# Kernel tuning notes

Hardware: AMD Instinct MI355X
Metric: run time of the kernel (lower is better)

Reference implementation:

```python
import jax, jax.numpy as jnp
import numpy as np

B, H, LB, PW, TC = 4096, 64, 32, 16, 1
WL = LB + PW  # window_length = look_back + prediction


def setup_inputs() -> dict:
    key = jax.random.key(0)
    ks = jax.random.split(key, 9)
    bnd = 1.0 / np.sqrt(H)  # torch Linear default init bound
    bnd_h = 1.0 / np.sqrt(H)
    return {
        "x": jax.random.normal(ks[0], (B, LB, TC), jnp.float32),
        "F_w": jax.random.uniform(ks[1], (WL, H, H), jnp.float32, -bnd, bnd),
        "F_b": jax.random.uniform(ks[2], (WL, H), jnp.float32, -bnd, bnd),
        "H_w": jax.random.uniform(ks[3], (WL, TC, H), jnp.float32, -bnd_h, bnd_h),
        "H_b": jax.random.uniform(ks[4], (WL, TC), jnp.float32, -bnd_h, bnd_h),
        "initial_state": jax.random.normal(ks[5], (H,), jnp.float32),
        "initial_covariance": 0.1 * jax.random.normal(ks[6], (H, H), jnp.float32),
        "Q": 0.1 * jax.random.normal(ks[7], (H, H), jnp.float32),
        "R": jnp.eye(TC, dtype=jnp.float32) + 0.1 * jax.random.normal(ks[8], (TC, TC), jnp.float32),
    }


def _kalman_forward(x, F_w, F_b, H_w, H_b, s0, P0, Q, R):
    nb = x.shape[0]
    hs = jnp.broadcast_to(s0, (nb, H))          # (B,H)
    P = jnp.broadcast_to(P0, (nb, H, H))        # (B,H,H)
    ys = jnp.moveaxis(x[:, :LB, :TC], 0, 1)     # (LB,B,TC) per-step observations

    @jax.checkpoint
    def kf_step(carry, inp):
        hs, P = carry
        Fw, Fb, Hw, Hb, y = inp
        hs_pred = hs @ Fw.T + Fb                                        # (B,H)
        P_pred = jnp.einsum('ij,bjk,lk->bil', Fw, P, Fw) + Q            # F P F^T + Q
        resid = y - (hs_pred @ Hw.T + Hb)                               # (B,TC)
        S = jnp.einsum('ij,bjk,lk->bil', Hw, P_pred, Hw) + R            # (B,TC,TC)
        K = jnp.einsum('bij,kj->bik', P_pred, Hw) @ jnp.linalg.inv(S)   # (B,H,TC)
        hs_new = hs_pred + jnp.einsum('bij,bj->bi', K, resid)
        P_new = P_pred - jnp.einsum('bit,tj,bjk->bik', K, Hw, P_pred)   # (I-KH)P_pred
        return (hs_new, P_new), None

    (hs, _), _ = jax.lax.scan(
        kf_step, (hs, P), (F_w[:LB], F_b[:LB], H_w[:LB], H_b[:LB], ys))

    def pred_step(hs, inp):
        Fw, Fb, Hw, Hb = inp
        hs = hs @ Fw.T + Fb
        return hs, hs @ Hw.T + Hb

    _, ems = jax.lax.scan(
        pred_step, hs, (F_w[LB:], F_b[LB:], H_w[LB:], H_b[LB:]))  # (PW,B,TC)
    # torch.cat(preds, dim=1).unsqueeze(-1) -> (B, PW*TC, 1)
    return jnp.moveaxis(ems, 0, 1).reshape(nb, PW * TC)[..., None]


def reference(x, F_w, F_b, H_w, H_b, initial_state, initial_covariance, Q, R):
    return _kalman_forward(x, F_w, F_b, H_w, H_b, initial_state, initial_covariance, Q, R)
```

## Files before the change

kernel.cpp:

```cpp
#include <hip/hip_runtime.h>


constexpr int KP_OFF = 0;
constexpr int WP_OFF = 2048;
constexpr int UP_OFF = 4160;
constexpr int EP_OFF = 5184;
constexpr int CNT_OFF = 5200;
constexpr int WS_U64 = 5201;

typedef float    f32x4 __attribute__((ext_vector_type(4)));
typedef _Float16 f16x4 __attribute__((ext_vector_type(4)));

#define MFMA16(a, b, c) __builtin_amdgcn_mfma_f32_16x16x16f16((a), (b), (c), 0, 0, 0)

template <int CTRL>
__device__ __forceinline__ float dpp_add(float x) {
  int v = __builtin_amdgcn_update_dpp(0, __builtin_bit_cast(int, x), CTRL, 0xf, 0xf, true);
  return x + __builtin_bit_cast(float, v);
}
__device__ __forceinline__ float sum16(float x) {
  x = dpp_add<0xB1>(x);
  x = dpp_add<0x4E>(x);
  x = dpp_add<0x141>(x);
  x = dpp_add<0x140>(x);
  return x;
}

__device__ __forceinline__ float spin_read(const unsigned long long* p, unsigned tag) {
  unsigned long long v = 0;
  for (int it = 0; it < (1 << 22); ++it) {
    v = __hip_atomic_load(p, __ATOMIC_RELAXED, __HIP_MEMORY_SCOPE_AGENT);
    if ((unsigned)(v >> 32) == tag) break;
  }
  union { unsigned u; float f; } cv; cv.u = (unsigned)v;
  return cv.f;
}
__device__ __forceinline__ float spin_read_sleep(const unsigned long long* p, unsigned tag) {
  unsigned long long v = 0;
  for (int it = 0; it < (1 << 20); ++it) {
    v = __hip_atomic_load(p, __ATOMIC_RELAXED, __HIP_MEMORY_SCOPE_AGENT);
    if ((unsigned)(v >> 32) == tag) break;
    __builtin_amdgcn_s_sleep(2);
  }
  union { unsigned u; float f; } cv; cv.u = (unsigned)v;
  return cv.f;
}
__device__ __forceinline__ void pub_write(unsigned long long* p, unsigned tag, float x) {
  union { float f; unsigned u; } cv; cv.f = x;
  __hip_atomic_store(p, ((unsigned long long)tag << 32) | cv.u,
                     __ATOMIC_RELAXED, __HIP_MEMORY_SCOPE_AGENT);
}
__device__ __forceinline__ void lds_barrier() {
  asm volatile("s_waitcnt lgkmcnt(0)" ::: "memory");
  __builtin_amdgcn_sched_barrier(0);
  __builtin_amdgcn_s_barrier();
  __builtin_amdgcn_sched_barrier(0);
}

__global__ __launch_bounds__(512) void kalman_fused(
    const float* __restrict__ Fw, const float* __restrict__ Fb,
    const float* __restrict__ Hw, const float* __restrict__ Hb,
    const float* __restrict__ s0, const float* __restrict__ P0,
    const float* __restrict__ Qg, const float* __restrict__ Rg,
    const float* __restrict__ x, float* __restrict__ out,
    unsigned long long* __restrict__ ws) {
  __shared__ __align__(16) char smem[43008];
  const int tid  = threadIdx.x;
  const int lane = tid & 63;
  const int w    = tid >> 6;
  const int blk  = blockIdx.x;
  unsigned long long* kp = ws + KP_OFF;
  unsigned long long* wp = ws + WP_OFF;
  unsigned long long* up = ws + UP_OFF;
  unsigned long long* ep = ws + EP_OFF;

  if (blk == 0) {
    _Float16* FFh = (_Float16*)smem;
    _Float16* TF  = (_Float16*)(smem + 8192);
    float*    PF  = (float*)(smem + 16384);
    float*    Hws = (float*)(smem + 32768);
    float*    nred = (float*)(smem + 40960);
    float*    mred = (float*)(smem + 41472);
    float*    Sred = (float*)(smem + 42496);

    const int l15 = lane & 15, g = lane >> 4;
    const int ti = w >> 1, half = w & 1;
    const int tj0 = 2 * half, tj1 = 2 * half + 1;
    const int sr = tid >> 3, sc0 = (tid & 7) * 8;
    const int fi0 = (sr >> 4) * 4 + (sc0 >> 4);
    const int L0  = (sr & 15) + 16 * ((sc0 & 15) >> 2);
    const float R0 = Rg[0];

    auto stageFh = [&](f32x4 a, f32x4 b) {
      f16x4 pa, pb;
      #pragma unroll
      for (int u = 0; u < 4; ++u) { pa[u] = (_Float16)a[u]; pb[u] = (_Float16)b[u]; }
      *(f16x4*)&FFh[(fi0 * 64 + L0) * 4]      = pa;
      *(f16x4*)&FFh[(fi0 * 64 + L0 + 16) * 4] = pb;
    };

    f32x4 qf0, qf1;
    #pragma unroll
    for (int reg = 0; reg < 4; ++reg) {
      qf0[reg] = Qg[(16 * ti + 4 * g + reg) * 64 + 16 * tj0 + l15];
      qf1[reg] = Qg[(16 * ti + 4 * g + reg) * 64 + 16 * tj1 + l15];
    }
    for (int idx = tid; idx < 2048; idx += 512) Hws[idx] = Hw[idx];
    #pragma unroll
    for (int s = 0; s < 2; ++s) {
      const int slot = tid + s * 512;
      const int f = slot >> 6, ln = slot & 63;
      const int a = f >> 2, b = f & 3, g2 = ln >> 4, l2 = ln & 15;
      f32x4 v;
      #pragma unroll
      for (int r = 0; r < 4; ++r)
        v[r] = P0[(16 * a + 4 * g2 + r) * 64 + 16 * b + l2];
      *(f32x4*)&PF[(f * 64 + ln) * 4] = v;
    }
    {
      f32x4 a = *(const f32x4*)(Fw + sr * 64 + sc0);
      f32x4 b = *(const f32x4*)(Fw + sr * 64 + sc0 + 4);
      stageFh(a, b);
    }
    for (int idx = tid; idx < 2 * 64; idx += 512) nred[idx] = 0.f;
    for (int idx = tid; idx < 4 * 64; idx += 512) mred[idx] = 0.f;
    if (tid < 8) Sred[tid] = 0.f;
    __syncthreads();

    f32x4 fna, fnb;
    for (int t = 0; t < 32; ++t) {
      if (t + 1 < 32) {
        fna = *(const f32x4*)(Fw + (size_t)(t + 1) * 4096 + sr * 64 + sc0);
        fnb = *(const f32x4*)(Fw + (size_t)(t + 1) * 4096 + sr * 64 + sc0 + 4);
      }
      float S;
      {
        const f32x4 sa = *(const f32x4*)&Sred[0];
        const f32x4 sb = *(const f32x4*)&Sred[4];
        S = ((sa.x + sa.y) + (sa.z + sa.w)) + ((sb.x + sb.y) + (sb.z + sb.w));
      }
      const float rcpS = 1.0f / (S + R0);
      const int ia = 16 * ti + l15;
      const float hPl = mred[ia] + mred[64 + ia] + mred[128 + ia] + mred[192 + ia];

      f16x4 Ah[4], Al[4];
      #pragma unroll
      for (int kc = 0; kc < 4; ++kc) {
        const int na = 16 * kc + 4 * g;
        const f32x4 n4 = *(const f32x4*)&nred[na] + *(const f32x4*)&nred[64 + na];
        const f32x4 k4 = n4 * rcpS;
        const f32x4 p4 = *(const f32x4*)&PF[((kc * 4 + ti) * 64 + lane) * 4] - k4 * hPl;
        #pragma unroll
        for (int j = 0; j < 4; ++j) {
          const _Float16 h_ = (_Float16)p4[j];
          Ah[kc][j] = h_;
          Al[kc][j] = (_Float16)((p4[j] - (float)h_) * 2048.0f);
        }
      }
      f16x4 Bf[2][4];
      #pragma unroll
      for (int s2 = 0; s2 < 2; ++s2) {
        const int tj = tj0 + s2;
        #pragma unroll
        for (int kc = 0; kc < 4; ++kc)
          Bf[s2][kc] = *(const f16x4*)&FFh[((tj * 4 + kc) * 64 + lane) * 4];
      }
      if (w == 0 && t > 0) {
        const float kl = (nred[lane] + nred[64 + lane]) * rcpS;
        pub_write(&kp[(t - 1) * 64 + lane], (unsigned)t, kl);
      }
      #pragma unroll
      for (int s2 = 0; s2 < 2; ++s2) {
        const int tj = tj0 + s2;
        f32x4 am = {0.f, 0.f, 0.f, 0.f}, a2 = {0.f, 0.f, 0.f, 0.f};
        #pragma unroll
        for (int kc = 0; kc < 4; ++kc) {
          am = MFMA16(Ah[kc], Bf[s2][kc], am);
          a2 = MFMA16(Al[kc], Bf[s2][kc], a2);
        }
        const f32x4 uv = am + a2 * (1.0f / 2048.0f);
        f16x4 uh;
        #pragma unroll
        for (int j = 0; j < 4; ++j) uh[j] = (_Float16)uv[j];
        *(f16x4*)&TF[((ti * 4 + tj) * 64 + lane) * 4] = uh;
      }
      lds_barrier();

      if (t + 1 < 32) stageFh(fna, fnb);
      f16x4 Ua[4];
      #pragma unroll
      for (int kc = 0; kc < 4; ++kc)
        Ua[kc] = *(const f16x4*)&TF[((kc * 4 + ti) * 64 + lane) * 4];
      f32x4 pout[2];
      #pragma unroll
      for (int s2 = 0; s2 < 2; ++s2) {
        const int tj = tj0 + s2;
        f32x4 acc = {0.f, 0.f, 0.f, 0.f};
        #pragma unroll
        for (int kc = 0; kc < 4; ++kc) acc = MFMA16(Ua[kc], Bf[s2][kc], acc);
        acc += (s2 ? qf1 : qf0);
        pout[s2] = acc;
        *(f32x4*)&PF[((ti * 4 + tj) * 64 + lane) * 4] = acc;
      }
      const float hcA = Hws[t * 64 + 16 * tj0 + l15];
      const float hcB = Hws[t * 64 + 16 * tj1 + l15];
      const f32x4 h4 = *(const f32x4*)&Hws[t * 64 + 16 * ti + 4 * g];
      const f32x4 npv = pout[0] * hcA + pout[1] * hcB;
      const float np0 = sum16(npv.x), np1 = sum16(npv.y);
      const float np2 = sum16(npv.z), np3 = sum16(npv.w);
      float sel = np0;
      sel = (l15 == 1) ? np1 : sel;
      sel = (l15 == 2) ? np2 : sel;
      sel = (l15 == 3) ? np3 : sel;
      if (l15 < 4) nred[half * 64 + 16 * ti + 4 * g + l15] = sel;
      float mp0 = pout[0].x * h4.x + pout[0].y * h4.y + pout[0].z * h4.z + pout[0].w * h4.w;
      float mp1 = pout[1].x * h4.x + pout[1].y * h4.y + pout[1].z * h4.z + pout[1].w * h4.w;
      mp0 += __shfl_xor(mp0, 16, 64); mp0 += __shfl_xor(mp0, 32, 64);
      mp1 += __shfl_xor(mp1, 16, 64); mp1 += __shfl_xor(mp1, 32, 64);
      if (g == 0) {
        mred[ti * 64 + 16 * tj0 + l15] = mp0;
        mred[ti * 64 + 16 * tj1 + l15] = mp1;
      }
      float sp = npv.x * h4.x + npv.y * h4.y + npv.z * h4.z + npv.w * h4.w;
      sp = sum16(sp);
      sp += __shfl_xor(sp, 16, 64); sp += __shfl_xor(sp, 32, 64);
      if (lane == 0) Sred[w] = sp;
      lds_barrier();
    }
    if (w == 0) {
      const f32x4 sa = *(const f32x4*)&Sred[0];
      const f32x4 sb = *(const f32x4*)&Sred[4];
      const float S = ((sa.x + sa.y) + (sa.z + sa.w)) + ((sb.x + sb.y) + (sb.z + sb.w));
      const float kl = (nred[lane] + nred[64 + lane]) / (S + R0);
      pub_write(&kp[31 * 64 + lane], 32u, kl);
    }
    return;
  }

  if (blk == 1) {
    for (int pi = 0; pi < 2; ++pi) {
      const int p = pi ? (15 - w) : w;
      const int q = 32 + p;
      float r = Hw[q * 64 + lane];
      float eacc = 0.f;
      for (int s = 0; s <= p; ++s) {
        const int m = q - s;
        eacc += r * Fb[m * 64 + lane];
        const float* Fm = Fw + (size_t)m * 4096;
        float r0 = 0.f, r1 = 0.f, r2 = 0.f, r3 = 0.f;
        for (int j = 0; j < 64; j += 4) {
          r0 += __shfl(r, j,     64) * Fm[j * 64 + lane];
          r1 += __shfl(r, j + 1, 64) * Fm[(j + 1) * 64 + lane];
          r2 += __shfl(r, j + 2, 64) * Fm[(j + 2) * 64 + lane];
          r3 += __shfl(r, j + 3, 64) * Fm[(j + 3) * 64 + lane];
        }
        r = (r0 + r1) + (r2 + r3);
      }
      eacc = sum16(eacc);
      eacc += __shfl_xor(eacc, 16, 64); eacc += __shfl_xor(eacc, 32, 64);
      pub_write(&up[p * 64 + lane], 1u, r);
      if (lane == 0) pub_write(&ep[p], 1u, eacc + Hb[q]);
    }
    __syncthreads();
    if (tid == 0)
      __hip_atomic_fetch_add(&ws[CNT_OFF], 1ull, __ATOMIC_RELAXED, __HIP_MEMORY_SCOPE_AGENT);
    return;
  }

  if (blk < 7) {
    float* vb = (float*)smem + w * 64;
    const int c = (blk - 2) * 8 + w;
    if (c > 32) return;
    if (c == 32) {
      pub_write(&wp[32 * 64 + lane], 1u, spin_read_sleep(&kp[31 * 64 + lane], 32u));
      if (lane == 0)
        __hip_atomic_fetch_add(&ws[CNT_OFF], 1ull, __ATOMIC_RELAXED, __HIP_MEMORY_SCOPE_AGENT);
      return;
    }
    const int t0 = (c == 0) ? 0 : c;
    float v = (c == 0) ? s0[lane] : spin_read_sleep(&kp[(c - 1) * 64 + lane], (unsigned)c);
    f32x4 fn[16];
    {
      const float* Fr = Fw + (size_t)t0 * 4096 + lane * 64;
      #pragma unroll
      for (int jc = 0; jc < 16; ++jc) fn[jc] = *(const f32x4*)(Fr + jc * 4);
    }
    float hn  = Hw[t0 * 64 + lane];
    float fbn = (c == 0) ? Fb[t0 * 64 + lane] : 0.f;
    for (int t = t0; t < 32; ++t) {
      vb[lane] = v;
      f32x4 fc[16];
      #pragma unroll
      for (int jc = 0; jc < 16; ++jc) fc[jc] = fn[jc];
      const float ht = hn, fbt = fbn;
      if (t + 1 < 32) {
        const float* Fr = Fw + (size_t)(t + 1) * 4096 + lane * 64;
        #pragma unroll
        for (int jc = 0; jc < 16; ++jc) fn[jc] = *(const f32x4*)(Fr + jc * 4);
        hn = Hw[(t + 1) * 64 + lane];
        if (c == 0) fbn = Fb[(t + 1) * 64 + lane];
      }
      float a0 = fbt, a1 = 0.f, a2 = 0.f, a3 = 0.f;
      #pragma unroll
      for (int jc = 0; jc < 16; ++jc) {
        const f32x4 vv = *(const f32x4*)(vb + jc * 4);
        a0 += fc[jc].x * vv.x; a1 += fc[jc].y * vv.y;
        a2 += fc[jc].z * vv.z; a3 += fc[jc].w * vv.w;
      }
      const float vp = (a0 + a1) + (a2 + a3);
      float hv = ht * vp;
      hv = sum16(hv);
      hv += __shfl_xor(hv, 16, 64); hv += __shfl_xor(hv, 32, 64);
      if (c == 0) hv += Hb[t];
      const float kt = spin_read_sleep(&kp[t * 64 + lane], (unsigned)(t + 1));
      v = vp - kt * hv;
    }
    pub_write(&wp[c * 64 + lane], 1u, v);
    if (lane == 0)
      __hip_atomic_fetch_add(&ws[CNT_OFF], 1ull, __ATOMIC_RELAXED, __HIP_MEMORY_SCOPE_AGENT);
    return;
  }

  {
    float* Ul = (float*)smem;
    float* Wl = (float*)(smem + 4352);
    float* Zl = (float*)(smem + 13328);
    float* El = (float*)(smem + 15504);
    const int b = (blk - 7) * 512 + tid;
    f32x4 xr[8];
    const f32x4* xp = (const f32x4*)(x + (size_t)b * 32);
    #pragma unroll
    for (int u = 0; u < 8; ++u) xr[u] = xp[u];

    if (tid == 0) {
      for (int it = 0; it < (1 << 20); ++it) {
        if (__hip_atomic_load(&ws[CNT_OFF], __ATOMIC_RELAXED, __HIP_MEMORY_SCOPE_AGENT) >= 34ull)
          break;
        __builtin_amdgcn_s_sleep(8);
      }
    }
    __syncthreads();
    for (int idx = tid; idx < 1024; idx += 512)
      Ul[(idx >> 6) * 68 + (idx & 63)] = spin_read(&up[idx], 1u);
    for (int idx = tid; idx < 2112; idx += 512)
      Wl[(idx >> 6) * 68 + (idx & 63)] = spin_read(&wp[idx], 1u);
    if (tid < 16) El[tid] = spin_read(&ep[tid], 1u);
    __syncthreads();
    for (int idx = tid; idx < 528; idx += 512) {
      const int p = idx / 33, cc = idx - p * 33;
      const float* Up = Ul + p * 68;
      const float* Wc = Wl + cc * 68;
      float a0 = 0.f, a1 = 0.f, a2 = 0.f, a3 = 0.f;
      #pragma unroll 4
      for (int i = 0; i < 64; i += 4) {
        a0 += Up[i] * Wc[i];         a1 += Up[i + 1] * Wc[i + 1];
        a2 += Up[i + 2] * Wc[i + 2]; a3 += Up[i + 3] * Wc[i + 3];
      }
      float z = (a0 + a1) + (a2 + a3);
      if (cc == 0) z += El[p];
      Zl[p * 34 + cc] = z;
    }
    __syncthreads();
    float acc[16];
    #pragma unroll
    for (int p = 0; p < 16; ++p) acc[p] = Zl[p * 34];
    #pragma unroll
    for (int u = 0; u < 8; ++u) {
      #pragma unroll
      for (int e = 0; e < 4; ++e) {
        const float xval = xr[u][e];
        const int t = u * 4 + e;
        #pragma unroll
        for (int p = 0; p < 16; ++p) acc[p] += Zl[p * 34 + 1 + t] * xval;
      }
    }
    float4* op = (float4*)(out + (size_t)b * 16);
    op[0] = make_float4(acc[0], acc[1], acc[2], acc[3]);
    op[1] = make_float4(acc[4], acc[5], acc[6], acc[7]);
    op[2] = make_float4(acc[8], acc[9], acc[10], acc[11]);
    op[3] = make_float4(acc[12], acc[13], acc[14], acc[15]);
  }
}

extern "C" void kernel_launch(void* const* d_in, const int* in_sizes, int n_in,
                              void* d_out, int out_size, void* d_ws, size_t ws_size,
                              hipStream_t stream) {
  (void)in_sizes; (void)n_in; (void)out_size; (void)ws_size;
  const float* x  = (const float*)d_in[0];
  const float* Fw = (const float*)d_in[1];
  const float* Fb = (const float*)d_in[2];
  const float* Hw = (const float*)d_in[3];
  const float* Hb = (const float*)d_in[4];
  const float* s0 = (const float*)d_in[5];
  const float* P0 = (const float*)d_in[6];
  const float* Q  = (const float*)d_in[7];
  const float* R  = (const float*)d_in[8];
  float* out = (float*)d_out;
  unsigned long long* ws = (unsigned long long*)d_ws;

  hipMemsetAsync(d_ws, 0, WS_U64 * sizeof(unsigned long long), stream);
  kalman_fused<<<15, 512, 0, stream>>>(Fw, Fb, Hw, Hb, s0, P0, Q, R, x, out, ws);
}
```

Baseline: 128.9 us.

## Run covariance recursion in a single wavefront with register-resident state

The covariance update in block 0 moves from eight wavefronts that exchange partial results through LDS with two barriers per step to one wavefront that keeps the full 64x64 P and F fragments in registers. This removes the per-step block barriers and LDS reductions on the serial critical path. In exchange a single wave issues all the MFMAs (four times the per-wave MFMA work) and register pressure rises sharply, which risks spills.

New measurement: 184.7 us. 1.43x slower.

```diff
diff --git a/kernel.cpp b/kernel.cpp
--- a/kernel.cpp
+++ b/kernel.cpp
@@ -49,12 +49,6 @@
   union { float f; unsigned u; } cv; cv.f = x;
   __hip_atomic_store(p, ((unsigned long long)tag << 32) | cv.u,
                      __ATOMIC_RELAXED, __HIP_MEMORY_SCOPE_AGENT);
-}
-__device__ __forceinline__ void lds_barrier() {
-  asm volatile("s_waitcnt lgkmcnt(0)" ::: "memory");
-  __builtin_amdgcn_sched_barrier(0);
-  __builtin_amdgcn_s_barrier();
-  __builtin_amdgcn_sched_barrier(0);
 }
 
 __global__ __launch_bounds__(512) void kalman_fused(
@@ -64,7 +58,7 @@
     const float* __restrict__ Qg, const float* __restrict__ Rg,
     const float* __restrict__ x, float* __restrict__ out,
     unsigned long long* __restrict__ ws) {
-  __shared__ __align__(16) char smem[43008];
+  __shared__ __align__(16) char smem[16896];
   const int tid  = threadIdx.x;
   const int lane = tid & 63;
   const int w    = tid >> 6;
@@ -75,164 +69,177 @@
   unsigned long long* ep = ws + EP_OFF;
 
   if (blk == 0) {
-    _Float16* FFh = (_Float16*)smem;
-    _Float16* TF  = (_Float16*)(smem + 8192);
-    float*    PF  = (float*)(smem + 16384);
-    float*    Hws = (float*)(smem + 32768);
-    float*    nred = (float*)(smem + 40960);
-    float*    mred = (float*)(smem + 41472);
-    float*    Sred = (float*)(smem + 42496);
-
+    float* QL = (float*)smem;
+    float* kL = (float*)(smem + 16384);
     const int l15 = lane & 15, g = lane >> 4;
-    const int ti = w >> 1, half = w & 1;
-    const int tj0 = 2 * half, tj1 = 2 * half + 1;
-    const int sr = tid >> 3, sc0 = (tid & 7) * 8;
-    const int fi0 = (sr >> 4) * 4 + (sc0 >> 4);
-    const int L0  = (sr & 15) + 16 * ((sc0 & 15) >> 2);
-    const float R0 = Rg[0];
-
-    auto stageFh = [&](f32x4 a, f32x4 b) {
-      f16x4 pa, pb;
-      #pragma unroll
-      for (int u = 0; u < 4; ++u) { pa[u] = (_Float16)a[u]; pb[u] = (_Float16)b[u]; }
-      *(f16x4*)&FFh[(fi0 * 64 + L0) * 4]      = pa;
-      *(f16x4*)&FFh[(fi0 * 64 + L0 + 16) * 4] = pb;
-    };
-
-    f32x4 qf0, qf1;
-    #pragma unroll
-    for (int reg = 0; reg < 4; ++reg) {
-      qf0[reg] = Qg[(16 * ti + 4 * g + reg) * 64 + 16 * tj0 + l15];
-      qf1[reg] = Qg[(16 * ti + 4 * g + reg) * 64 + 16 * tj1 + l15];
-    }
-    for (int idx = tid; idx < 2048; idx += 512) Hws[idx] = Hw[idx];
-    #pragma unroll
-    for (int s = 0; s < 2; ++s) {
-      const int slot = tid + s * 512;
+
+    for (int slot = tid; slot < 1024; slot += 512) {
       const int f = slot >> 6, ln = slot & 63;
       const int a = f >> 2, b = f & 3, g2 = ln >> 4, l2 = ln & 15;
       f32x4 v;
       #pragma unroll
       for (int r = 0; r < 4; ++r)
-        v[r] = P0[(16 * a + 4 * g2 + r) * 64 + 16 * b + l2];
-      *(f32x4*)&PF[(f * 64 + ln) * 4] = v;
+        v[r] = Qg[(16 * a + 4 * g2 + r) * 64 + 16 * b + l2];
+      *(f32x4*)&QL[slot * 4] = v;
+    }
+    __syncthreads();
+    if (w != 0) return;
+
+    const float R0 = Rg[0];
+    f32x4 PF[4][4];
+    #pragma unroll
+    for (int a = 0; a < 4; ++a)
+      #pragma unroll
+      for (int b = 0; b < 4; ++b)
+        #pragma unroll
+        for (int r = 0; r < 4; ++r)
+          PF[a][b][r] = P0[(16 * a + 4 * g + r) * 64 + 16 * b + l15];
+    f16x4 Fh[4][4];
+    #pragma unroll
+    for (int a = 0; a < 4; ++a)
+      #pragma unroll
+      for (int b = 0; b < 4; ++b) {
+        const f32x4 v = *(const f32x4*)(Fw + (16 * a + l15) * 64 + 16 * b + 4 * g);
+        f16x4 hf;
+        #pragma unroll
+        for (int j = 0; j < 4; ++j) hf[j] = (_Float16)v[j];
+        Fh[a][b] = hf;
+      }
+    f32x4 hrow[4];
+    float hcol[4];
+    #pragma unroll
+    for (int a = 0; a < 4; ++a) hrow[a] = *(const f32x4*)(Hw + 16 * a + 4 * g);
+    #pragma unroll
+    for (int b = 0; b < 4; ++b) hcol[b] = Hw[16 * b + l15];
+
+    f32x4 numf[4];
+    float hpc[4] = {0.f, 0.f, 0.f, 0.f};
+    float Sv = 0.f;
+    #pragma unroll
+    for (int a = 0; a < 4; ++a) numf[a] = (f32x4){0.f, 0.f, 0.f, 0.f};
+
+    for (int t = 0; t < 32; ++t) {
+      const float rcpS = 1.0f / (Sv + R0);
+      f32x4 krow[4];
+      #pragma unroll
+      for (int a = 0; a < 4; ++a) krow[a] = numf[a] * rcpS;
+      if (t > 0 && l15 == 0) {
+        #pragma unroll
+        for (int a = 0; a < 4; ++a) *(f32x4*)&kL[16 * a + 4 * g] = krow[a];
+      }
+      f16x4 Ah[4][4], Al[4][4];
+      #pragma unroll
+      for (int a = 0; a < 4; ++a)
+        #pragma unroll
+        for (int b = 0; b < 4; ++b) {
+          const f32x4 p = PF[a][b] - krow[a] * hpc[b];
+          f16x4 hi_, lo_;
+          #pragma unroll
+          for (int j = 0; j < 4; ++j) {
+            const _Float16 h_ = (_Float16)p[j];
+            hi_[j] = h_;
+            lo_[j] = (_Float16)((p[j] - (float)h_) * 2048.0f);
+          }
+          Ah[a][b] = hi_;
+          Al[a][b] = lo_;
+        }
+      f16x4 Uh[4][4];
+      #pragma unroll
+      for (int ti = 0; ti < 4; ++ti)
+        #pragma unroll
+        for (int tj = 0; tj < 4; ++tj) {
+          f32x4 am = {0.f, 0.f, 0.f, 0.f}, a2 = {0.f, 0.f, 0.f, 0.f};
+          #pragma unroll
+          for (int kc = 0; kc < 4; ++kc) {
+            am = MFMA16(Ah[kc][ti], Fh[tj][kc], am);
+            a2 = MFMA16(Al[kc][ti], Fh[tj][kc], a2);
+          }
+          const f32x4 u = am + a2 * (1.0f / 2048.0f);
+          f16x4 uh;
+          #pragma unroll
+          for (int j = 0; j < 4; ++j) uh[j] = (_Float16)u[j];
+          Uh[ti][tj] = uh;
+        }
+      if (t > 0) pub_write(&kp[(t - 1) * 64 + lane], (unsigned)t, kL[lane]);
+      f32x4 Fn[4][4], hrowN[4];
+      float hcolN[4];
+      if (t + 1 < 32) {
+        const float* Fbase = Fw + (size_t)(t + 1) * 4096;
+        #pragma unroll
+        for (int a = 0; a < 4; ++a)
+          #pragma unroll
+          for (int b = 0; b < 4; ++b)
+            Fn[a][b] = *(const f32x4*)(Fbase + (16 * a + l15) * 64 + 16 * b + 4 * g);
+        #pragma unroll
+        for (int a = 0; a < 4; ++a)
+          hrowN[a] = *(const f32x4*)(Hw + (t + 1) * 64 + 16 * a + 4 * g);
+        #pragma unroll
+        for (int b = 0; b < 4; ++b) hcolN[b] = Hw[(t + 1) * 64 + 16 * b + l15];
+      }
+      #pragma unroll
+      for (int ti = 0; ti < 4; ++ti)
+        #pragma unroll
+        for (int tj = 0; tj < 4; ++tj) {
+          f32x4 acc = *(const f32x4*)&QL[((ti * 4 + tj) * 64 + lane) * 4];
+          #pragma unroll
+          for (int kc = 0; kc < 4; ++kc)
+            acc = MFMA16(Uh[kc][ti], Fh[tj][kc], acc);
+          PF[ti][tj] = acc;
+        }
+      #pragma unroll
+      for (int a = 0; a < 4; ++a) {
+        f32x4 np = PF[a][0] * hcol[0] + PF[a][1] * hcol[1] +
+                   PF[a][2] * hcol[2] + PF[a][3] * hcol[3];
+        #pragma unroll
+        for (int r = 0; r < 4; ++r) np[r] = sum16(np[r]);
+        numf[a] = np;
+      }
+      #pragma unroll
+      for (int b = 0; b < 4; ++b) {
+        float hp = 0.f;
+        #pragma unroll
+        for (int a = 0; a < 4; ++a) {
+          const f32x4 tv = hrow[a] * PF[a][b];
+          hp += (tv.x + tv.y) + (tv.z + tv.w);
+        }
+        hp += __shfl_xor(hp, 16, 64);
+        hp += __shfl_xor(hp, 32, 64);
+        hpc[b] = hp;
+      }
+      {
+        float sp = 0.f;
+        #pragma unroll
+        for (int a = 0; a < 4; ++a) {
+          const f32x4 tv = hrow[a] * numf[a];
+          sp += (tv.x + tv.y) + (tv.z + tv.w);
+        }
+        sp += __shfl_xor(sp, 16, 64);
+        sp += __shfl_xor(sp, 32, 64);
+        Sv = sp;
+      }
+      if (t + 1 < 32) {
+        #pragma unroll
+        for (int a = 0; a < 4; ++a) {
+          #pragma unroll
+          for (int b = 0; b < 4; ++b) {
+            f16x4 hf;
+            #pragma unroll
+            for (int j = 0; j < 4; ++j) hf[j] = (_Float16)Fn[a][b][j];
+            Fh[a][b] = hf;
+          }
+          hrow[a] = hrowN[a];
+        }
+        #pragma unroll
+        for (int b = 0; b < 4; ++b) hcol[b] = hcolN[b];
+      }
     }
     {
-      f32x4 a = *(const f32x4*)(Fw + sr * 64 + sc0);
-      f32x4 b = *(const f32x4*)(Fw + sr * 64 + sc0 + 4);
-      stageFh(a, b);
-    }
-    for (int idx = tid; idx < 2 * 64; idx += 512) nred[idx] = 0.f;
-    for (int idx = tid; idx < 4 * 64; idx += 512) mred[idx] = 0.f;
-    if (tid < 8) Sred[tid] = 0.f;
-    __syncthreads();
-
-    f32x4 fna, fnb;
-    for (int t = 0; t < 32; ++t) {
-      if (t + 1 < 32) {
-        fna = *(const f32x4*)(Fw + (size_t)(t + 1) * 4096 + sr * 64 + sc0);
-        fnb = *(const f32x4*)(Fw + (size_t)(t + 1) * 4096 + sr * 64 + sc0 + 4);
-      }
-      float S;
-      {
-        const f32x4 sa = *(const f32x4*)&Sred[0];
-        const f32x4 sb = *(const f32x4*)&Sred[4];
-        S = ((sa.x + sa.y) + (sa.z + sa.w)) + ((sb.x + sb.y) + (sb.z + sb.w));
-      }
-      const float rcpS = 1.0f / (S + R0);
-      const int ia = 16 * ti + l15;
-      const float hPl = mred[ia] + mred[64 + ia] + mred[128 + ia] + mred[192 + ia];
-
-      f16x4 Ah[4], Al[4];
-      #pragma unroll
-      for (int kc = 0; kc < 4; ++kc) {
-        const int na = 16 * kc + 4 * g;
-        const f32x4 n4 = *(const f32x4*)&nred[na] + *(const f32x4*)&nred[64 + na];
-        const f32x4 k4 = n4 * rcpS;
-        const f32x4 p4 = *(const f32x4*)&PF[((kc * 4 + ti) * 64 + lane) * 4] - k4 * hPl;
-        #pragma unroll
-        for (int j = 0; j < 4; ++j) {
-          const _Float16 h_ = (_Float16)p4[j];
-          Ah[kc][j] = h_;
-          Al[kc][j] = (_Float16)((p4[j] - (float)h_) * 2048.0f);
-        }
-      }
-      f16x4 Bf[2][4];
-      #pragma unroll
-      for (int s2 = 0; s2 < 2; ++s2) {
-        const int tj = tj0 + s2;
-        #pragma unroll
-        for (int kc = 0; kc < 4; ++kc)
-          Bf[s2][kc] = *(const f16x4*)&FFh[((tj * 4 + kc) * 64 + lane) * 4];
-      }
-      if (w == 0 && t > 0) {
-        const float kl = (nred[lane] + nred[64 + lane]) * rcpS;
-        pub_write(&kp[(t - 1) * 64 + lane], (unsigned)t, kl);
-      }
-      #pragma unroll
-      for (int s2 = 0; s2 < 2; ++s2) {
-        const int tj = tj0 + s2;
-        f32x4 am = {0.f, 0.f, 0.f, 0.f}, a2 = {0.f, 0.f, 0.f, 0.f};
-        #pragma unroll
-        for (int kc = 0; kc < 4; ++kc) {
-          am = MFMA16(Ah[kc], Bf[s2][kc], am);
-          a2 = MFMA16(Al[kc], Bf[s2][kc], a2);
-        }
-        const f32x4 uv = am + a2 * (1.0f / 2048.0f);
-        f16x4 uh;
-        #pragma unroll
-        for (int j = 0; j < 4; ++j) uh[j] = (_Float16)uv[j];
-        *(f16x4*)&TF[((ti * 4 + tj) * 64 + lane) * 4] = uh;
-      }
-      lds_barrier();
-
-      if (t + 1 < 32) stageFh(fna, fnb);
-      f16x4 Ua[4];
-      #pragma unroll
-      for (int kc = 0; kc < 4; ++kc)
-        Ua[kc] = *(const f16x4*)&TF[((kc * 4 + ti) * 64 + lane) * 4];
-      f32x4 pout[2];
-      #pragma unroll
-      for (int s2 = 0; s2 < 2; ++s2) {
-        const int tj = tj0 + s2;
-        f32x4 acc = {0.f, 0.f, 0.f, 0.f};
-        #pragma unroll
-        for (int kc = 0; kc < 4; ++kc) acc = MFMA16(Ua[kc], Bf[s2][kc], acc);
-        acc += (s2 ? qf1 : qf0);
-        pout[s2] = acc;
-        *(f32x4*)&PF[((ti * 4 + tj) * 64 + lane) * 4] = acc;
-      }
-      const float hcA = Hws[t * 64 + 16 * tj0 + l15];
-      const float hcB = Hws[t * 64 + 16 * tj1 + l15];
-      const f32x4 h4 = *(const f32x4*)&Hws[t * 64 + 16 * ti + 4 * g];
-      const f32x4 npv = pout[0] * hcA + pout[1] * hcB;
-      const float np0 = sum16(npv.x), np1 = sum16(npv.y);
-      const float np2 = sum16(npv.z), np3 = sum16(npv.w);
-      float sel = np0;
-      sel = (l15 == 1) ? np1 : sel;
-      sel = (l15 == 2) ? np2 : sel;
-      sel = (l15 == 3) ? np3 : sel;
-      if (l15 < 4) nred[half * 64 + 16 * ti + 4 * g + l15] = sel;
-      float mp0 = pout[0].x * h4.x + pout[0].y * h4.y + pout[0].z * h4.z + pout[0].w * h4.w;
-      float mp1 = pout[1].x * h4.x + pout[1].y * h4.y + pout[1].z * h4.z + pout[1].w * h4.w;
-      mp0 += __shfl_xor(mp0, 16, 64); mp0 += __shfl_xor(mp0, 32, 64);
-      mp1 += __shfl_xor(mp1, 16, 64); mp1 += __shfl_xor(mp1, 32, 64);
-      if (g == 0) {
-        mred[ti * 64 + 16 * tj0 + l15] = mp0;
-        mred[ti * 64 + 16 * tj1 + l15] = mp1;
-      }
-      float sp = npv.x * h4.x + npv.y * h4.y + npv.z * h4.z + npv.w * h4.w;
-      sp = sum16(sp);
-      sp += __shfl_xor(sp, 16, 64); sp += __shfl_xor(sp, 32, 64);
-      if (lane == 0) Sred[w] = sp;
-      lds_barrier();
-    }
-    if (w == 0) {
-      const f32x4 sa = *(const f32x4*)&Sred[0];
-      const f32x4 sb = *(const f32x4*)&Sred[4];
-      const float S = ((sa.x + sa.y) + (sa.z + sa.w)) + ((sb.x + sb.y) + (sb.z + sb.w));
-      const float kl = (nred[lane] + nred[64 + lane]) / (S + R0);
-      pub_write(&kp[31 * 64 + lane], 32u, kl);
+      const float rcpS = 1.0f / (Sv + R0);
+      if (l15 == 0) {
+        #pragma unroll
+        for (int a = 0; a < 4; ++a) *(f32x4*)&kL[16 * a + 4 * g] = numf[a] * rcpS;
+      }
+      pub_write(&kp[31 * 64 + lane], 32u, kL[lane]);
     }
     return;
   }
```
